# Optimization experiments

Hardware: AMD Instinct MI355X
Metric: run time of the kernel (lower is better)

Reference implementation:

```python
import jax, jax.numpy as jnp
import numpy as np

D_MODEL = 1024
NHEAD = 16
HEAD_DIM = D_MODEL // NHEAD
B, S = 4, 2048
NEG_INF = -1000000000.0


def setup_inputs() -> dict:
    key = jax.random.key(0)
    ks = jax.random.split(key, 12)
    s = 1.0 / np.sqrt(D_MODEL)
    inp = {
        "query": jax.random.normal(ks[0], (B, S, D_MODEL), jnp.float32),
        "key": jax.random.normal(ks[1], (B, S, D_MODEL), jnp.float32),
        "value": jax.random.normal(ks[2], (B, S, D_MODEL), jnp.float32),
        # causal mask: 1 = attend, 0 = blocked
        "mask": jnp.broadcast_to(jnp.tril(jnp.ones((S, S), jnp.int32)), (B, S, S)),
        "Wq": jax.random.normal(ks[3], (D_MODEL, D_MODEL), jnp.float32) * s,
        "bq": jnp.zeros((D_MODEL,), jnp.float32),
        "Wk": jax.random.normal(ks[4], (D_MODEL, D_MODEL), jnp.float32) * s,
        "bk": jnp.zeros((D_MODEL,), jnp.float32),
        "Wv": jax.random.normal(ks[5], (D_MODEL, D_MODEL), jnp.float32) * s,
        "bv": jnp.zeros((D_MODEL,), jnp.float32),
        "Wo": jax.random.normal(ks[6], (D_MODEL, D_MODEL), jnp.float32) * s,
        "bo": jnp.zeros((D_MODEL,), jnp.float32),
    }
    return inp


def reference(query, key, value, mask, Wq, bq, Wk, bk, Wv, bv, Wo, bo):
    b, sq, d = query.shape
    scale = np.float32(1.0 / np.sqrt(HEAD_DIM))

    def proj(x, W, bias):
        # nn.Linear: x @ W.T + b, then split heads -> [b, H, s, hd]
        y = jnp.einsum('bsd,ed->bse', x, W) + bias
        return y.reshape(b, -1, NHEAD, HEAD_DIM).transpose(0, 2, 1, 3)

    q = proj(query, Wq, bq)
    k = proj(key, Wk, bk)
    v = proj(value, Wv, bv)

    scores = jnp.einsum('bhqd,bhkd->bhqk', q, k) * scale  # [b,H,sq,sk]
    scores = jnp.where(mask[:, None, :, :] == 0, jnp.float32(NEG_INF), scores)
    attn = jax.nn.softmax(scores, axis=-1)  # dropout p=0 -> identity
    out = jnp.einsum('bhqk,bhkd->bhqd', attn, v)
    out = out.transpose(0, 2, 1, 3).reshape(b, sq, d)
    return jnp.einsum('bsd,ed->bse', out, Wo) + bo
```

## Files before the change

### kernel.cpp

```cpp
#include <hip/hip_runtime.h>
#include <stdint.h>

#define D_MODEL 1024
#define NHEAD   16
#define BATCH   4
#define SEQ     2048
#define M_TOTAL 8192
#define R_ELEMS ((size_t)M_TOTAL * D_MODEL)
#define W_ELEMS ((size_t)D_MODEL * D_MODEL)

typedef short bf8_t __attribute__((ext_vector_type(8)));
typedef float f4_t  __attribute__((ext_vector_type(4)));

#define MFMA16(a, b, c) __builtin_amdgcn_mfma_f32_16x16x32_bf16(a, b, c, 0, 0, 0)

#define SCALE_LOG2E 0.1803368801111244f

__device__ __forceinline__ unsigned short f2b(float f) {
    union { float f; unsigned int u; } v; v.f = f;
    return (unsigned short)((v.u + 0x7fffu + ((v.u >> 16) & 1u)) >> 16);
}
__device__ __forceinline__ unsigned short f2b_fast(float f) {
    union { float f; unsigned int u; } v; v.f = f;
    return (unsigned short)((v.u + 0x8000u) >> 16);
}

#if __has_builtin(__builtin_amdgcn_exp2f)
#define EXP2(x) __builtin_amdgcn_exp2f(x)
#else
#define EXP2(x) exp2f(x)
#endif

__device__ __forceinline__ void async16(const unsigned short* g, unsigned short* l) {
    __builtin_amdgcn_global_load_lds(
        (const __attribute__((address_space(1))) unsigned int*)g,
        (__attribute__((address_space(3))) unsigned int*)l, 16, 0, 0);
}

__device__ __forceinline__ void cvt_store8(const float* __restrict__ g, unsigned short* l) {
    const float4 x = *(const float4*)g;
    const float4 y = *(const float4*)(g + 4);
    unsigned short t[8] = { f2b(x.x), f2b(x.y), f2b(x.z), f2b(x.w),
                            f2b(y.x), f2b(y.y), f2b(y.z), f2b(y.w) };
    *(uint4*)l = *(const uint4*)t;
}

template <int CTRL>
__device__ __forceinline__ float dppf(float x) {
    return __int_as_float(__builtin_amdgcn_mov_dpp(__float_as_int(x), CTRL, 0xf, 0xf, true));
}
__device__ __forceinline__ float rowmax16(float v) {
    v = fmaxf(v, dppf<0xB1>(v));
    v = fmaxf(v, dppf<0x4E>(v));
    v = fmaxf(v, dppf<0x141>(v));
    v = fmaxf(v, dppf<0x140>(v));
    return v;
}
__device__ __forceinline__ float rowsum16(float v) {
    v += dppf<0xB1>(v);
    v += dppf<0x4E>(v);
    v += dppf<0x141>(v);
    v += dppf<0x140>(v);
    return v;
}

struct CvtArgs { const float* s[7]; unsigned short* d[7]; };

__global__ __launch_bounds__(256)
void cvt_multi(CvtArgs a) {
    const unsigned int gid = blockIdx.x * 256 + threadIdx.x;
    unsigned int t, i;
    if (gid < (3u << 20)) { t = gid >> 20; i = gid & ((1u << 20) - 1); }
    else { const unsigned int g = gid - (3u << 20); t = 3 + (g >> 17); i = g & ((1u << 17) - 1); }
    const float* s = a.s[t] + (size_t)i * 8;
    unsigned short* d = a.d[t] + (size_t)i * 8;
    const float4 x = *(const float4*)s;
    const float4 y = *(const float4*)(s + 4);
    unsigned short o[8] = { f2b(x.x), f2b(x.y), f2b(x.z), f2b(x.w),
                            f2b(y.x), f2b(y.y), f2b(y.z), f2b(y.w) };
    *(uint4*)d = *(const uint4*)o;
}

template<int WF32>
__device__ __forceinline__ void gemm_tile(const unsigned short* __restrict__ A,
                                          const void* __restrict__ Wp,
                                          const float* __restrict__ bias,
                                          void* __restrict__ outv,
                                          const int ol, const int m0, const int n0,
                                          unsigned short* As, unsigned short* Bs)
{
    const int tid  = threadIdx.x;
    const int lane = tid & 63;
    const int wave = tid >> 6;
    const int quad = lane >> 4;
    const int l16  = lane & 15;
    const int wm = (wave >> 1) * 64;
    const int wn = (wave & 1) * 64;

    f4_t acc[4][4];
#pragma unroll
    for (int i = 0; i < 4; ++i)
#pragma unroll
        for (int j = 0; j < 4; ++j)
            acc[i][j] = (f4_t){0.f, 0.f, 0.f, 0.f};

    for (int k0 = 0; k0 < 1024; k0 += 32) {
#pragma unroll
        for (int i = 0; i < 2; ++i) {
            const int s = tid + i * 256;
            const int r = s >> 2;
            const int c = (s & 3) ^ ((r >> 1) & 3);
            async16(A + (size_t)(m0 + r) * 1024 + k0 + c * 8, &As[s * 8]);
            if (WF32)
                cvt_store8((const float*)Wp + (size_t)(n0 + r) * 1024 + k0 + c * 8, &Bs[s * 8]);
            else
                async16((const unsigned short*)Wp + (size_t)(n0 + r) * 1024 + k0 + c * 8, &Bs[s * 8]);
        }
        __syncthreads();

        bf8_t af[4], bf[4];
#pragma unroll
        for (int mt = 0; mt < 4; ++mt) {
            const int rr = wm + mt * 16 + l16;
            af[mt] = *(const bf8_t*)&As[(rr * 4 + (quad ^ ((rr >> 1) & 3))) * 8];
        }
#pragma unroll
        for (int nt = 0; nt < 4; ++nt) {
            const int rr = wn + nt * 16 + l16;
            bf[nt] = *(const bf8_t*)&Bs[(rr * 4 + (quad ^ ((rr >> 1) & 3))) * 8];
        }
#pragma unroll
        for (int mt = 0; mt < 4; ++mt)
#pragma unroll
            for (int nt = 0; nt < 4; ++nt)
                acc[mt][nt] = MFMA16(af[mt], bf[nt], acc[mt][nt]);
        __syncthreads();
    }

#pragma unroll
    for (int mt = 0; mt < 4; ++mt) {
#pragma unroll
        for (int nt = 0; nt < 4; ++nt) {
            const int nn = n0 + wn + nt * 16 + l16;
            const float bv = bias[nn];
            const int mbase = m0 + wm + mt * 16 + quad * 4;
            if (ol == 2) {
                float* of = (float*)outv;
#pragma unroll
                for (int r = 0; r < 4; ++r)
                    of[(size_t)(mbase + r) * 1024 + nn] = acc[mt][nt][r] + bv;
            } else if (ol == 0) {
                unsigned short* ob = (unsigned short*)outv;
                const int h = nn >> 6, d = nn & 63;
#pragma unroll
                for (int r = 0; r < 4; ++r) {
                    const int m = mbase + r;
                    const int b = m >> 11, s2 = m & 2047;
                    ob[((size_t)((b * 16 + h) * 2048 + s2) << 6) + d] = f2b(acc[mt][nt][r] + bv);
                }
            } else {
                unsigned short* ob = (unsigned short*)outv;
                const int h = nn >> 6, d = nn & 63;
                const int b = mbase >> 11, s2 = mbase & 2047;
                unsigned short pk[4];
#pragma unroll
                for (int r = 0; r < 4; ++r) pk[r] = f2b(acc[mt][nt][r] + bv);
                *(uint2*)&ob[((size_t)((b * 16 + h) * 64 + d) << 11) + s2] = *(const uint2*)pk;
            }
        }
    }
}

template<int WF32>
__global__ __launch_bounds__(256, 2)
void qkv_gemm(const unsigned short* __restrict__ qb, const unsigned short* __restrict__ kb,
              const unsigned short* __restrict__ vb,
              const void* __restrict__ Wq, const void* __restrict__ Wk, const void* __restrict__ Wv,
              const float* __restrict__ bq, const float* __restrict__ bk, const float* __restrict__ bv,
              unsigned short* __restrict__ Qh, unsigned short* __restrict__ Kh,
              unsigned short* __restrict__ Vt)
{
    __shared__ unsigned short As[128 * 32];
    __shared__ unsigned short Bs[128 * 32];
    const int z = blockIdx.z;
    const unsigned short* A = (z == 0) ? qb : (z == 1) ? kb : vb;
    const void* W  = (z == 0) ? Wq : (z == 1) ? Wk : Wv;
    const float* bias = (z == 0) ? bq : (z == 1) ? bk : bv;
    void* out = (z == 0) ? (void*)Qh : (z == 1) ? (void*)Kh : (void*)Vt;
    gemm_tile<WF32>(A, W, bias, out, (z == 2) ? 1 : 0,
                    blockIdx.y * 128, blockIdx.x * 128, As, Bs);
}

template<int WF32>
__global__ __launch_bounds__(256, 2)
void o_gemm(const unsigned short* __restrict__ ctx, const void* __restrict__ Wo,
            const float* __restrict__ bo, float* __restrict__ out)
{
    __shared__ unsigned short As[128 * 32];
    __shared__ unsigned short Bs[128 * 32];
    gemm_tile<WF32>(ctx, Wo, bo, out, 2, blockIdx.y * 128, blockIdx.x * 128, As, Bs);
}

__global__ __launch_bounds__(256, 2)
void attn_kernel(const unsigned short* __restrict__ Qh,
                 const unsigned short* __restrict__ Kh,
                 const unsigned short* __restrict__ Vt,
                 unsigned short* __restrict__ ctx)
{
    __shared__ unsigned short Ks[64 * 64];
    __shared__ unsigned short Vs[64 * 64];
    __shared__ unsigned short Pw[8][16 * 72];

    const int tid  = threadIdx.x;
    const int lane = tid & 63;
    const int wave = tid >> 6;
    const int quad = lane >> 4;
    const int l16  = lane & 15;

    const int bid = blockIdx.x;
    const int bh  = bid & 63;
    const int jg  = bid >> 6;
    const int j   = jg * 4 + wave;

    const int qrow0[2] = { j * 16, (127 - j) * 16 };
    const int nkt[2] = { (qrow0[0] + 79) >> 6, (qrow0[1] + 79) >> 6 };
    const int nktmax = ((127 - jg * 4) * 16 + 79) >> 6;

    bf8_t qf0[2], qf1[2];
#pragma unroll
    for (int s = 0; s < 2; ++s) {
        const unsigned short* qa = Qh + ((size_t)(bh * SEQ + qrow0[s] + l16) << 6);
        qf0[s] = *(const bf8_t*)(qa + quad * 8);
        qf1[s] = *(const bf8_t*)(qa + 32 + quad * 8);
    }

    float mrow[2][4], lrow[2][4];
    f4_t oacc[2][4];
#pragma unroll
    for (int s = 0; s < 2; ++s)
#pragma unroll
        for (int r = 0; r < 4; ++r) {
            mrow[s][r] = -1e30f; lrow[s][r] = 0.f;
            oacc[s][r] = (f4_t){0.f, 0.f, 0.f, 0.f};
        }

    for (int kt = 0; kt < nktmax; ++kt) {
        const int kb = kt * 64;

#pragma unroll
        for (int i2 = 0; i2 < 2; ++i2) {
            const int s = tid + i2 * 256;
            const int r = s >> 3;
            const int c = (s & 7) ^ (r & 7);
            async16(Kh + ((size_t)(bh * SEQ + kb + r) << 6) + c * 8, &Ks[s * 8]);
            async16(Vt + ((size_t)(bh * 64 + r) << 11) + kb + c * 8, &Vs[s * 8]);
        }
        __syncthreads();

#pragma unroll
        for (int s = 1; s >= 0; --s) {
            if (kt >= nkt[s]) continue;
            f4_t sacc[4];
#pragma unroll
            for (int nb = 0; nb < 4; ++nb) {
                const int rr = nb * 16 + l16;
                const bf8_t kf0 = *(const bf8_t*)&Ks[(rr * 8 + (quad ^ (rr & 7))) * 8];
                const bf8_t kf1 = *(const bf8_t*)&Ks[(rr * 8 + ((quad + 4) ^ (rr & 7))) * 8];
                f4_t sc = (f4_t){0.f, 0.f, 0.f, 0.f};
                sc = MFMA16(qf0[s], kf0, sc);
                sc = MFMA16(qf1[s], kf1, sc);
                sacc[nb] = sc;
            }
            const bool diag = (kt == nkt[s] - 1);
            float sv[4][4];
#pragma unroll
            for (int nb = 0; nb < 4; ++nb) {
                const int kcol = kb + nb * 16 + l16;
#pragma unroll
                for (int r = 0; r < 4; ++r) {
                    const float x = sacc[nb][r] * SCALE_LOG2E;
                    sv[nb][r] = (!diag || kcol <= qrow0[s] + quad * 4 + r) ? x : -1e30f;
                }
            }
#pragma unroll
            for (int r = 0; r < 4; ++r) {
                float v = fmaxf(fmaxf(sv[0][r], sv[1][r]), fmaxf(sv[2][r], sv[3][r]));
                v = rowmax16(v);
                const float mnew = fmaxf(mrow[s][r], v);
                const float alpha = EXP2(mrow[s][r] - mnew);
                mrow[s][r] = mnew;
                float rs = 0.f;
#pragma unroll
                for (int nb = 0; nb < 4; ++nb) {
                    sv[nb][r] = EXP2(sv[nb][r] - mnew);
                    rs += sv[nb][r];
                }
                rs = rowsum16(rs);
                lrow[s][r] = alpha * lrow[s][r] + rs;
#pragma unroll
                for (int d4 = 0; d4 < 4; ++d4)
                    oacc[s][d4][r] *= alpha;
            }
            unsigned short* pws = &Pw[wave * 2 + s][0];
#pragma unroll
            for (int nb = 0; nb < 4; ++nb)
#pragma unroll
                for (int r = 0; r < 4; ++r)
                    pws[(quad * 4 + r) * 72 + nb * 16 + l16] = f2b_fast(sv[nb][r]);

            asm volatile("s_waitcnt lgkmcnt(0)" ::: "memory");

            const bf8_t pf0 = *(const bf8_t*)&pws[l16 * 72 + quad * 8];
            const bf8_t pf1 = *(const bf8_t*)&pws[l16 * 72 + 32 + quad * 8];
#pragma unroll
            for (int d4 = 0; d4 < 4; ++d4) {
                const int rr = d4 * 16 + l16;
                const bf8_t vfa = *(const bf8_t*)&Vs[(rr * 8 + (quad ^ (rr & 7))) * 8];
                const bf8_t vfb = *(const bf8_t*)&Vs[(rr * 8 + ((quad + 4) ^ (rr & 7))) * 8];
                oacc[s][d4] = MFMA16(pf0, vfa, oacc[s][d4]);
                oacc[s][d4] = MFMA16(pf1, vfb, oacc[s][d4]);
            }
        }
        __syncthreads();
    }

    const int b = bh >> 4, h = bh & 15;
#pragma unroll
    for (int s = 0; s < 2; ++s)
#pragma unroll
        for (int r = 0; r < 4; ++r) {
            const float inv = 1.f / lrow[s][r];
            const int qr = qrow0[s] + quad * 4 + r;
            unsigned short* cb = ctx + ((size_t)(b * SEQ + qr) << 10) + h * 64;
#pragma unroll
            for (int d4 = 0; d4 < 4; ++d4)
                cb[d4 * 16 + l16] = f2b(oacc[s][d4][r] * inv);
        }
}

extern "C" void kernel_launch(void* const* d_in, const int* in_sizes, int n_in,
                              void* d_out, int out_size, void* d_ws, size_t ws_size,
                              hipStream_t stream) {
    const float* q_in = (const float*)d_in[0];
    const float* k_in = (const float*)d_in[1];
    const float* v_in = (const float*)d_in[2];
    const float* Wq = (const float*)d_in[4];
    const float* bq = (const float*)d_in[5];
    const float* Wk = (const float*)d_in[6];
    const float* bk = (const float*)d_in[7];
    const float* Wv = (const float*)d_in[8];
    const float* bv = (const float*)d_in[9];
    const float* Wo = (const float*)d_in[10];
    const float* bo = (const float*)d_in[11];

    unsigned short* w  = (unsigned short*)d_ws;
    unsigned short* Qh = w;
    unsigned short* Kh = w + R_ELEMS;
    unsigned short* Vt = w + 2 * R_ELEMS;
    unsigned short* X  = w + 3 * R_ELEMS;
    unsigned short* qb = (unsigned short*)d_out;
    unsigned short* kb = qb + R_ELEMS;

    const dim3 gb(256);
    const size_t need_big = (4 * R_ELEMS + 4 * W_ELEMS) * 2;

    CvtArgs ca;
    ca.s[0] = q_in; ca.d[0] = qb;
    ca.s[1] = k_in; ca.d[1] = kb;
    ca.s[2] = v_in; ca.d[2] = X;

    if (ws_size >= need_big) {
        unsigned short* wb = w + 4 * R_ELEMS;
        ca.s[3] = Wq; ca.d[3] = wb;
        ca.s[4] = Wk; ca.d[4] = wb + W_ELEMS;
        ca.s[5] = Wv; ca.d[5] = wb + 2 * W_ELEMS;
        ca.s[6] = Wo; ca.d[6] = wb + 3 * W_ELEMS;
        cvt_multi<<<14336, gb, 0, stream>>>(ca);
        qkv_gemm<0><<<dim3(8, 64, 3), gb, 0, stream>>>(qb, kb, X, wb, wb + W_ELEMS,
                                                       wb + 2 * W_ELEMS, bq, bk, bv, Qh, Kh, Vt);
        attn_kernel<<<dim3(1024), gb, 0, stream>>>(Qh, Kh, Vt, X);
        o_gemm<0><<<dim3(8, 64), gb, 0, stream>>>(X, wb + 3 * W_ELEMS, bo, (float*)d_out);
    } else {
        ca.s[3] = Wq; ca.d[3] = qb;
        ca.s[4] = Wk; ca.d[4] = qb;
        ca.s[5] = Wv; ca.d[5] = qb;
        ca.s[6] = Wo; ca.d[6] = qb;
        cvt_multi<<<12288, gb, 0, stream>>>(ca);
        qkv_gemm<1><<<dim3(8, 64, 3), gb, 0, stream>>>(qb, kb, X, Wq, Wk, Wv,
                                                       bq, bk, bv, Qh, Kh, Vt);
        attn_kernel<<<dim3(1024), gb, 0, stream>>>(Qh, Kh, Vt, X);
        o_gemm<1><<<dim3(8, 64), gb, 0, stream>>>(X, Wo, bo, (float*)d_out);
    }
}
```

Measured before the change: 397.3 us.

## Fold softmax scale into Q projection, lazy rescale, MFMA row sums, swizzled P buffer

The softmax scale times log2(e) is now applied in the Q projection epilogue, so the attention loop no longer multiplies each score. The running max is updated and the accumulators rescaled only when some row's new max exceeds the stored one by more than 8 (log2 domain). This bounds unnormalized exponentials by 2^8. Row sums come from an MFMA of P against a ones vector instead of DPP reductions, and the P scratch buffer drops its padding for an XOR-swizzled layout. Risks: Q is rounded to bf16 after scaling, and bf16 probabilities above 1 lose some precision in both numerator and denominator.

```diff
diff --git a/kernel.cpp b/kernel.cpp
--- a/kernel.cpp
+++ b/kernel.cpp
@@ -54,13 +54,6 @@
     v = fmaxf(v, dppf<0x4E>(v));
     v = fmaxf(v, dppf<0x141>(v));
     v = fmaxf(v, dppf<0x140>(v));
-    return v;
-}
-__device__ __forceinline__ float rowsum16(float v) {
-    v += dppf<0xB1>(v);
-    v += dppf<0x4E>(v);
-    v += dppf<0x141>(v);
-    v += dppf<0x140>(v);
     return v;
 }
 
@@ -87,7 +80,8 @@
                                           const float* __restrict__ bias,
                                           void* __restrict__ outv,
                                           const int ol, const int m0, const int n0,
-                                          unsigned short* As, unsigned short* Bs)
+                                          unsigned short* As, unsigned short* Bs,
+                                          const float oscale)
 {
     const int tid  = threadIdx.x;
     const int lane = tid & 63;
@@ -148,7 +142,7 @@
                 float* of = (float*)outv;
 #pragma unroll
                 for (int r = 0; r < 4; ++r)
-                    of[(size_t)(mbase + r) * 1024 + nn] = acc[mt][nt][r] + bv;
+                    of[(size_t)(mbase + r) * 1024 + nn] = (acc[mt][nt][r] + bv) * oscale;
             } else if (ol == 0) {
                 unsigned short* ob = (unsigned short*)outv;
                 const int h = nn >> 6, d = nn & 63;
@@ -156,7 +150,8 @@
                 for (int r = 0; r < 4; ++r) {
                     const int m = mbase + r;
                     const int b = m >> 11, s2 = m & 2047;
-                    ob[((size_t)((b * 16 + h) * 2048 + s2) << 6) + d] = f2b(acc[mt][nt][r] + bv);
+                    ob[((size_t)((b * 16 + h) * 2048 + s2) << 6) + d] =
+                        f2b((acc[mt][nt][r] + bv) * oscale);
                 }
             } else {
                 unsigned short* ob = (unsigned short*)outv;
@@ -164,7 +159,7 @@
                 const int b = mbase >> 11, s2 = mbase & 2047;
                 unsigned short pk[4];
 #pragma unroll
-                for (int r = 0; r < 4; ++r) pk[r] = f2b(acc[mt][nt][r] + bv);
+                for (int r = 0; r < 4; ++r) pk[r] = f2b((acc[mt][nt][r] + bv) * oscale);
                 *(uint2*)&ob[((size_t)((b * 16 + h) * 64 + d) << 11) + s2] = *(const uint2*)pk;
             }
         }
@@ -188,7 +183,8 @@
     const float* bias = (z == 0) ? bq : (z == 1) ? bk : bv;
     void* out = (z == 0) ? (void*)Qh : (z == 1) ? (void*)Kh : (void*)Vt;
     gemm_tile<WF32>(A, W, bias, out, (z == 2) ? 1 : 0,
-                    blockIdx.y * 128, blockIdx.x * 128, As, Bs);
+                    blockIdx.y * 128, blockIdx.x * 128, As, Bs,
+                    (z == 0) ? SCALE_LOG2E : 1.0f);
 }
 
 template<int WF32>
@@ -198,7 +194,7 @@
 {
     __shared__ unsigned short As[128 * 32];
     __shared__ unsigned short Bs[128 * 32];
-    gemm_tile<WF32>(ctx, Wo, bo, out, 2, blockIdx.y * 128, blockIdx.x * 128, As, Bs);
+    gemm_tile<WF32>(ctx, Wo, bo, out, 2, blockIdx.y * 128, blockIdx.x * 128, As, Bs, 1.0f);
 }
 
 __global__ __launch_bounds__(256, 2)
@@ -209,7 +205,7 @@
 {
     __shared__ unsigned short Ks[64 * 64];
     __shared__ unsigned short Vs[64 * 64];
-    __shared__ unsigned short Pw[8][16 * 72];
+    __shared__ unsigned short Pw[8][16 * 64];
 
     const int tid  = threadIdx.x;
     const int lane = tid & 63;
@@ -226,6 +222,9 @@
     const int nkt[2] = { (qrow0[0] + 79) >> 6, (qrow0[1] + 79) >> 6 };
     const int nktmax = ((127 - jg * 4) * 16 + 79) >> 6;
 
+    const short ob = (short)0x3F80;
+    const bf8_t ONESV = { ob, ob, ob, ob, ob, ob, ob, ob };
+
     bf8_t qf0[2], qf1[2];
 #pragma unroll
     for (int s = 0; s < 2; ++s) {
@@ -234,15 +233,18 @@
         qf1[s] = *(const bf8_t*)(qa + 32 + quad * 8);
     }
 
-    float mrow[2][4], lrow[2][4];
+    float mrow[2][4];
+    f4_t lacc[2];
     f4_t oacc[2][4];
 #pragma unroll
-    for (int s = 0; s < 2; ++s)
+    for (int s = 0; s < 2; ++s) {
+        lacc[s] = (f4_t){0.f, 0.f, 0.f, 0.f};
 #pragma unroll
         for (int r = 0; r < 4; ++r) {
-            mrow[s][r] = -1e30f; lrow[s][r] = 0.f;
+            mrow[s][r] = -1e30f;
             oacc[s][r] = (f4_t){0.f, 0.f, 0.f, 0.f};
         }
+    }
 
     for (int kt = 0; kt < nktmax; ++kt) {
         const int kb = kt * 64;
@@ -272,46 +274,55 @@
                 sacc[nb] = sc;
             }
             const bool diag = (kt == nkt[s] - 1);
-            float sv[4][4];
+            if (diag) {
+#pragma unroll
+                for (int nb = 0; nb < 4; ++nb) {
+                    const int kcol = kb + nb * 16 + l16;
+#pragma unroll
+                    for (int r = 0; r < 4; ++r)
+                        if (kcol > qrow0[s] + quad * 4 + r) sacc[nb][r] = -1e30f;
+                }
+            }
+            float vmax[4];
+            float g = -1e30f;
+#pragma unroll
+            for (int r = 0; r < 4; ++r) {
+                float v = fmaxf(fmaxf(sacc[0][r], sacc[1][r]),
+                                fmaxf(sacc[2][r], sacc[3][r]));
+                v = rowmax16(v);
+                vmax[r] = v;
+                g = fmaxf(g, v - mrow[s][r]);
+            }
+            if (__any(g > 8.0f)) {
+#pragma unroll
+                for (int r = 0; r < 4; ++r) {
+                    const float mnew = fmaxf(mrow[s][r], vmax[r]);
+                    const float alpha = EXP2(mrow[s][r] - mnew);
+                    mrow[s][r] = mnew;
+                    lacc[s][r] *= alpha;
+#pragma unroll
+                    for (int d4 = 0; d4 < 4; ++d4)
+                        oacc[s][d4][r] *= alpha;
+                }
+            }
+            unsigned short* pws = &Pw[wave * 2 + s][0];
 #pragma unroll
             for (int nb = 0; nb < 4; ++nb) {
-                const int kcol = kb + nb * 16 + l16;
+                const int ch0 = nb * 2 + (l16 >> 3);
 #pragma unroll
                 for (int r = 0; r < 4; ++r) {
-                    const float x = sacc[nb][r] * SCALE_LOG2E;
-                    sv[nb][r] = (!diag || kcol <= qrow0[s] + quad * 4 + r) ? x : -1e30f;
+                    const int row = quad * 4 + r;
+                    const float p = EXP2(sacc[nb][r] - mrow[s][r]);
+                    pws[row * 64 + (((ch0 ^ (row & 7))) << 3) + (l16 & 7)] = f2b_fast(p);
                 }
             }
-#pragma unroll
-            for (int r = 0; r < 4; ++r) {
-                float v = fmaxf(fmaxf(sv[0][r], sv[1][r]), fmaxf(sv[2][r], sv[3][r]));
-                v = rowmax16(v);
-                const float mnew = fmaxf(mrow[s][r], v);
-                const float alpha = EXP2(mrow[s][r] - mnew);
-                mrow[s][r] = mnew;
-                float rs = 0.f;
-#pragma unroll
-                for (int nb = 0; nb < 4; ++nb) {
-                    sv[nb][r] = EXP2(sv[nb][r] - mnew);
-                    rs += sv[nb][r];
-                }
-                rs = rowsum16(rs);
-                lrow[s][r] = alpha * lrow[s][r] + rs;
-#pragma unroll
-                for (int d4 = 0; d4 < 4; ++d4)
-                    oacc[s][d4][r] *= alpha;
-            }
-            unsigned short* pws = &Pw[wave * 2 + s][0];
-#pragma unroll
-            for (int nb = 0; nb < 4; ++nb)
-#pragma unroll
-                for (int r = 0; r < 4; ++r)
-                    pws[(quad * 4 + r) * 72 + nb * 16 + l16] = f2b_fast(sv[nb][r]);
 
             asm volatile("s_waitcnt lgkmcnt(0)" ::: "memory");
 
-            const bf8_t pf0 = *(const bf8_t*)&pws[l16 * 72 + quad * 8];
-            const bf8_t pf1 = *(const bf8_t*)&pws[l16 * 72 + 32 + quad * 8];
+            const bf8_t pf0 = *(const bf8_t*)&pws[(l16 * 8 + (quad ^ (l16 & 7))) * 8];
+            const bf8_t pf1 = *(const bf8_t*)&pws[(l16 * 8 + ((quad + 4) ^ (l16 & 7))) * 8];
+            lacc[s] = MFMA16(pf0, ONESV, lacc[s]);
+            lacc[s] = MFMA16(pf1, ONESV, lacc[s]);
 #pragma unroll
             for (int d4 = 0; d4 < 4; ++d4) {
                 const int rr = d4 * 16 + l16;
@@ -329,7 +340,7 @@
     for (int s = 0; s < 2; ++s)
 #pragma unroll
         for (int r = 0; r < 4; ++r) {
-            const float inv = 1.f / lrow[s][r];
+            const float inv = 1.f / lacc[s][r];
             const int qr = qrow0[s] + quad * 4 + r;
             unsigned short* cb = ctx + ((size_t)(b * SEQ + qr) << 10) + h * 64;
 #pragma unroll
```

Result: faster. 381.7 us (-3.9%).
